# Performance work log

Measured on AMD Instinct MI355X. Metric: run time of the kernel, lower is better.

The kernel has to match this reference:

```python
import jax, jax.numpy as jnp
import numpy as np

B, S, C, V, LAT, NL = 256, 512, 256, 32, 256, 7
DILS = [1, 2, 4, 8, 16, 32, 64]
EPS = 1e-5


def setup_inputs() -> dict:
    key = jax.random.key(0)
    ks = jax.random.split(key, 24)
    s = 0.05
    inp = {
        "x": jax.random.randint(ks[0], (B, S), 0, V, dtype=jnp.int64 if jax.config.read("jax_enable_x64") else jnp.int32),
        "z": jax.random.normal(ks[1], (B, LAT), dtype=jnp.float32),
        "emb": jax.random.normal(ks[2], (V, C), dtype=jnp.float32) * s,
        "latent_W": jax.random.normal(ks[3], (LAT, C), dtype=jnp.float32) * s,
        "latent_b": jnp.zeros((C,), jnp.float32),
        "ln1_g": jnp.ones((NL, C), jnp.float32),
        "ln1_b": jnp.zeros((NL, C), jnp.float32),
        "w1": jax.random.normal(ks[4], (NL, C, C), jnp.float32) * s,
        "b1": jnp.zeros((NL, C), jnp.float32),
        "ln2_g": jnp.ones((NL, C), jnp.float32),
        "ln2_b": jnp.zeros((NL, C), jnp.float32),
        "wd": jax.random.normal(ks[5], (NL, 2, C, C), jnp.float32) * s,  # tap 0 = x[t-d], tap 1 = x[t]
        "bd": jnp.zeros((NL, C), jnp.float32),
        "ln3_g": jnp.ones((NL, C), jnp.float32),
        "ln3_b": jnp.zeros((NL, C), jnp.float32),
        "we": jax.random.normal(ks[6], (NL, C, C), jnp.float32) * s,
        "be": jnp.zeros((NL, C), jnp.float32),
        "wg": jax.random.normal(ks[7], (NL, C, C), jnp.float32) * s,
        "bg": jnp.zeros((NL, C), jnp.float32),
        "out_W": jax.random.normal(ks[8], (C, V), jnp.float32) * s,
        "out_b": jnp.zeros((V,), jnp.float32),
    }
    return inp


def _ln(h, g, b):
    mu = h.mean(-1, keepdims=True)
    var = jnp.mean((h - mu) ** 2, axis=-1, keepdims=True)
    return (h - mu) * jax.lax.rsqrt(var + EPS) * g + b


def _lrelu(h):
    return jnp.where(h >= 0, h, 0.01 * h)


def reference(x, z, emb, latent_W, latent_b, ln1_g, ln1_b, w1, b1,
              ln2_g, ln2_b, wd, bd, ln3_g, ln3_b, we, be, wg, bg,
              out_W, out_b):
    # channel-last layout [B, S, C] throughout (fuses away the torch transposes)
    h = emb[x] + (z @ latent_W + latent_b)[:, None, :]
    for i, d in enumerate(DILS):
        x_inp = h
        t = _lrelu(_ln(x_inp, ln1_g[i], ln1_b[i]))
        t = t @ w1[i] + b1[i]
        t = _lrelu(_ln(t, ln2_g[i], ln2_b[i]))
        # causal dilated conv, kernel=2: out[t] = W0*x[t-d] + W1*x[t]
        t_shift = jnp.pad(t, ((0, 0), (d, 0), (0, 0)))[:, :t.shape[1], :]
        t = t_shift @ wd[i, 0] + t @ wd[i, 1] + bd[i]
        t = _lrelu(_ln(t, ln3_g[i], ln3_b[i]))
        gated = (t @ we[i] + be[i]) * jax.nn.sigmoid(t @ wg[i] + bg[i])
        h = gated + x_inp
    logits = h @ out_W + out_b                      # [B, S, V]
    lp = jax.nn.log_softmax(logits, axis=-1)
    # gather log-prob of next token: lp[:, :-1, :] at x[:, 1:]
    return jnp.take_along_axis(lp[:, :-1, :], x[:, 1:, None], axis=2)[..., 0]
```

## Files before the change

### kernel.cpp

```cpp
#include <hip/hip_runtime.h>

typedef unsigned short u16;
typedef unsigned int   u32;
typedef __attribute__((ext_vector_type(8))) short short8;
typedef __attribute__((ext_vector_type(4))) float f32x4;

struct __align__(8) u16x4 { u16 x, y, z, w; };

#define NL 7
#define M_DIM 131072

#define VMW(N) asm volatile("s_waitcnt vmcnt(" #N ")" ::: "memory")
#define LGW()  asm volatile("s_waitcnt lgkmcnt(0)" ::: "memory")
#define BAR()  __builtin_amdgcn_s_barrier()

__device__ __forceinline__ float b2f(u16 u) {
  union { float f; u32 i; } c; c.i = ((u32)u) << 16; return c.f;
}
__device__ __forceinline__ u16 f2b(float f) {
  union { float f; u32 i; } c; c.f = f;
  u32 r = c.i + 0x7FFFu + ((c.i >> 16) & 1u);
  return (u16)(r >> 16);
}
__device__ __forceinline__ void gload16(const void* g, void* l) {
  __builtin_amdgcn_global_load_lds((const __attribute__((address_space(1))) void*)g,
                                   (__attribute__((address_space(3))) void*)l, 16, 0, 0);
}
__device__ __forceinline__ int xIdx(int row, int chunk) {
  return row * 256 + (((chunk) ^ (row & 7)) << 3);
}


__global__ __launch_bounds__(256) void conv_w1_k(const float* __restrict__ w1, u16* __restrict__ wT) {
  int idx = blockIdx.x * 256 + threadIdx.x;
  int i = idx >> 16, rem = idx & 65535;
  int n = rem >> 8, k = rem & 255;
  wT[idx] = f2b(w1[(i << 16) + (k << 8) + n]);
}

__global__ __launch_bounds__(256) void conv_wd_k(const float* __restrict__ wd, u16* __restrict__ wT) {
  int idx = blockIdx.x * 256 + threadIdx.x;
  int i = idx / 131072, rem = idx & 131071;
  int n = rem >> 9, k2 = rem & 511;
  int tap = k2 >> 8, k = k2 & 255;
  wT[idx] = f2b(wd[(((i * 2 + tap) << 8) + k) * 256 + n]);
}

__global__ __launch_bounds__(256) void conv_weg_k(const float* __restrict__ we, const float* __restrict__ wg,
                                                  u16* __restrict__ wT) {
  int idx = blockIdx.x * 256 + threadIdx.x;
  int i = idx / 131072, rem = idx & 131071;
  int src = rem >> 16, n = (rem >> 8) & 255, k = rem & 255;
  const float* W = src ? wg : we;
  wT[idx] = f2b(W[((i << 8) + k) * 256 + n]);
}

__global__ __launch_bounds__(256) void conv_wo_k(const float* __restrict__ outW, u16* __restrict__ wTo) {
  int idx = blockIdx.x * 256 + threadIdx.x;
  int v = idx >> 8, k = idx & 255;
  wTo[idx] = f2b(outW[k * 32 + v]);
}


__global__ __launch_bounds__(256) void zlat_k(const float* __restrict__ z, const float* __restrict__ W,
                                              const float* __restrict__ bias, float* __restrict__ zlat) {
  int b = blockIdx.x, c = threadIdx.x;
  float acc = bias[c];
  for (int l = 0; l < 256; ++l) acc += z[b * 256 + l] * W[l * 256 + c];
  zlat[b * 256 + c] = acc;
}


__global__ __launch_bounds__(256) void embed_k(const int* __restrict__ x, const float* __restrict__ emb,
                                               const float* __restrict__ zlat, u16* __restrict__ h) {
  int wave = threadIdx.x >> 6, lane = threadIdx.x & 63;
  int r = blockIdx.x * 4 + wave;
  int c = lane * 4;
  int tok = x[r];
  int bi = r >> 9;
  float4 ev = *(const float4*)&emb[tok * 256 + c];
  float4 zv = *(const float4*)&zlat[bi * 256 + c];
  u16x4 hb;
  hb.x = f2b(ev.x + zv.x); hb.y = f2b(ev.y + zv.y);
  hb.z = f2b(ev.z + zv.z); hb.w = f2b(ev.w + zv.w);
  *(u16x4*)&h[(long)r * 256 + c] = hb;
}


__global__ __launch_bounds__(256, 3) void gemm1_k(
    const u16* __restrict__ h, const u16* __restrict__ WT,
    const float* __restrict__ ln1g, const float* __restrict__ ln1b,
    const float* __restrict__ bias,
    const float* __restrict__ ln2g, const float* __restrict__ ln2b,
    u16* __restrict__ V)
{
  __shared__ __align__(16) u16 lA[64 * 256];
  __shared__ __align__(16) u16 lB[256 * 32];
  float* pS  = (float*)lB;
  float* pQ  = (float*)(lB + 512);
  float* muA = (float*)(lB + 1024);
  float* rsA = (float*)(lB + 1152);
  const int tid = threadIdx.x;
  const int lane = tid & 63;
  const int wv = tid >> 6;
  const int wc = wv * 64;
  const int m0 = blockIdx.x * 64;
  const int rA = tid >> 2;
  const int cSw = ((((tid & 3) - ((tid >> 3) & 3)) & 3)) * 8;
  const int lr = lane & 15;
  const int quad = lane >> 4;
  const int sw = ((quad + ((lr >> 1) & 3)) & 3) * 8;

  {
    const int half = lane >> 5, l5 = lane & 31;
    float4 ga = *(const float4*)&ln1g[l5 * 8];
    float4 gb = *(const float4*)&ln1g[l5 * 8 + 4];
    float4 ba = *(const float4*)&ln1b[l5 * 8];
    float4 bb = *(const float4*)&ln1b[l5 * 8 + 4];
    #pragma unroll 4
    for (int it = 0; it < 8; ++it) {
      int row = wv * 16 + it * 2 + half;
      uint4 hv = *(const uint4*)(h + (long)(m0 + row) * 256 + l5 * 8);
      float v0 = b2f((u16)(hv.x & 0xffff)), v1 = b2f((u16)(hv.x >> 16));
      float v2 = b2f((u16)(hv.y & 0xffff)), v3 = b2f((u16)(hv.y >> 16));
      float v4 = b2f((u16)(hv.z & 0xffff)), v5 = b2f((u16)(hv.z >> 16));
      float v6 = b2f((u16)(hv.w & 0xffff)), v7 = b2f((u16)(hv.w >> 16));
      float s = v0 + v1 + v2 + v3 + v4 + v5 + v6 + v7;
      float q = v0*v0 + v1*v1 + v2*v2 + v3*v3 + v4*v4 + v5*v5 + v6*v6 + v7*v7;
      #pragma unroll
      for (int o = 1; o < 32; o <<= 1) { s += __shfl_xor(s, o); q += __shfl_xor(q, o); }
      float mu = s * 0.00390625f;
      float var = q * 0.00390625f - mu * mu;
      float rs = rsqrtf(var + 1e-5f);
      float y0 = (v0 - mu) * rs * ga.x + ba.x; y0 = y0 >= 0.f ? y0 : 0.01f * y0;
      float y1 = (v1 - mu) * rs * ga.y + ba.y; y1 = y1 >= 0.f ? y1 : 0.01f * y1;
      float y2 = (v2 - mu) * rs * ga.z + ba.z; y2 = y2 >= 0.f ? y2 : 0.01f * y2;
      float y3 = (v3 - mu) * rs * ga.w + ba.w; y3 = y3 >= 0.f ? y3 : 0.01f * y3;
      float y4 = (v4 - mu) * rs * gb.x + bb.x; y4 = y4 >= 0.f ? y4 : 0.01f * y4;
      float y5 = (v5 - mu) * rs * gb.y + bb.y; y5 = y5 >= 0.f ? y5 : 0.01f * y5;
      float y6 = (v6 - mu) * rs * gb.z + bb.z; y6 = y6 >= 0.f ? y6 : 0.01f * y6;
      float y7 = (v7 - mu) * rs * gb.w + bb.w; y7 = y7 >= 0.f ? y7 : 0.01f * y7;
      uint4 ov;
      ov.x = (u32)f2b(y0) | ((u32)f2b(y1) << 16);
      ov.y = (u32)f2b(y2) | ((u32)f2b(y3) << 16);
      ov.z = (u32)f2b(y4) | ((u32)f2b(y5) << 16);
      ov.w = (u32)f2b(y6) | ((u32)f2b(y7) << 16);
      *(uint4*)&lA[xIdx(row, l5)] = ov;
    }
  }

  f32x4 acc[4][4];
  #pragma unroll
  for (int i = 0; i < 4; ++i)
    #pragma unroll
    for (int j = 0; j < 4; ++j) {
      acc[i][j][0] = 0.f; acc[i][j][1] = 0.f; acc[i][j][2] = 0.f; acc[i][j][3] = 0.f;
    }

  for (int kt = 0; kt < 8; ++kt) {
    const long bofs = (long)rA * 256 + kt * 32 + cSw;
    #pragma unroll
    for (int j = 0; j < 4; ++j)
      gload16(WT + bofs + (long)(64 * j) * 256, &lB[tid * 8 + j * 2048]);
    __syncthreads();

    short8 af[4], bfr[4];
    #pragma unroll
    for (int mt = 0; mt < 4; ++mt)
      af[mt] = *(const short8*)&lA[xIdx(mt * 16 + lr, 4 * kt + quad)];
    #pragma unroll
    for (int nt = 0; nt < 4; ++nt)
      bfr[nt] = *(const short8*)&lB[(wc + nt * 16 + lr) * 32 + sw];
    #pragma unroll
    for (int mt = 0; mt < 4; ++mt)
      #pragma unroll
      for (int nt = 0; nt < 4; ++nt)
        acc[mt][nt] = __builtin_amdgcn_mfma_f32_16x16x32_bf16(af[mt], bfr[nt], acc[mt][nt], 0, 0, 0);
    __syncthreads();
  }

  float biasv[4], gv[4], bv[4];
  #pragma unroll
  for (int nt = 0; nt < 4; ++nt) {
    int n = wc + nt * 16 + lr;
    biasv[nt] = bias[n]; gv[nt] = ln2g[n]; bv[nt] = ln2b[n];
  }
  #pragma unroll
  for (int mt = 0; mt < 4; ++mt)
    #pragma unroll
    for (int r = 0; r < 4; ++r) {
      float s = 0.f, q = 0.f;
      #pragma unroll
      for (int nt = 0; nt < 4; ++nt) {
        float v = acc[mt][nt][r] + biasv[nt];
        acc[mt][nt][r] = v;
        s += v; q += v * v;
      }
      #pragma unroll
      for (int o = 1; o < 16; o <<= 1) { s += __shfl_xor(s, o); q += __shfl_xor(q, o); }
      if (lr == 0) { pS[(mt * 16 + quad * 4 + r) * 4 + wv] = s; pQ[(mt * 16 + quad * 4 + r) * 4 + wv] = q; }
    }
  __syncthreads();
  if (tid < 64) {
    float S = pS[tid * 4 + 0] + pS[tid * 4 + 1] + pS[tid * 4 + 2] + pS[tid * 4 + 3];
    float Q = pQ[tid * 4 + 0] + pQ[tid * 4 + 1] + pQ[tid * 4 + 2] + pQ[tid * 4 + 3];
    float mu = S * 0.00390625f;
    float var = Q * 0.00390625f - mu * mu;
    muA[tid] = mu; rsA[tid] = rsqrtf(var + 1e-5f);
  }
  __syncthreads();
  #pragma unroll
  for (int mt = 0; mt < 4; ++mt)
    #pragma unroll
    for (int r = 0; r < 4; ++r) {
      int row = mt * 16 + quad * 4 + r;
      float mu = muA[row], rs = rsA[row];
      #pragma unroll
      for (int nt = 0; nt < 4; ++nt) {
        float y = (acc[mt][nt][r] - mu) * rs * gv[nt] + bv[nt];
        y = y >= 0.f ? y : 0.01f * y;
        V[(long)(m0 + row) * 256 + wc + nt * 16 + lr] = f2b(y);
      }
    }
}


__global__ __launch_bounds__(512, 2) void conv_gate_k(
    const u16* __restrict__ A,
    const u16* __restrict__ WTd,
    int dil,
    const float* __restrict__ bd3, const float* __restrict__ g3, const float* __restrict__ bb3,
    const u16* __restrict__ WTe, const u16* __restrict__ WTg,
    const float* __restrict__ bev_, const float* __restrict__ bgv_,
    u16* __restrict__ h)
{
  __shared__ __align__(16) u16 pT[128 * 256];
  __shared__ __align__(16) u16 stg[2][12288];
  float* pS  = (float*)stg[0];
  float* pQ  = (float*)(stg[0] + 1024);
  float* muA = (float*)(stg[0] + 2048);
  float* rsA = (float*)(stg[0] + 2304);

  const int tid = threadIdx.x;
  const int lane = tid & 63;
  const int wv = tid >> 6;
  const int mw = wv >> 2;
  const int nw = wv & 3;
  const int rb = mw * 64;
  const int wc = nw * 64;
  const int m0 = blockIdx.x * 128;
  const int rA = tid >> 2;
  const int cSw = ((((tid & 3) - ((tid >> 3) & 3)) & 3)) * 8;
  const int lr = lane & 15;
  const int quad = lane >> 4;
  const int sw = ((quad + ((lr >> 1) & 3)) & 3) * 8;
  const int mm = m0 + rA;
  const int s1 = mm & 511;
  const short8 zero8 = {0, 0, 0, 0, 0, 0, 0, 0};

  bool zz[4];
  #pragma unroll
  for (int mt = 0; mt < 4; ++mt)
    zz[mt] = ((m0 + rb + mt * 16 + lr) & 511) < dil;

#define STAGE1(KT, BB) do {                                                   \
    const int kt_ = (KT);                                                     \
    const int kk_ = (kt_ & 7) * 32;                                           \
    const int rr_ = (kt_ < 8 && s1 >= dil) ? (mm - dil) : mm;                 \
    gload16(A + (long)rr_ * 256 + kk_ + cSw, &stg[BB][tid * 8]);              \
    const u16* bS_ = WTd + kt_ * 32 + cSw;                                    \
    gload16(bS_ + (long)rA * 512,         &stg[BB][4096 + tid * 8]);          \
    gload16(bS_ + (long)(rA + 128) * 512, &stg[BB][8192 + tid * 8]);          \
  } while (0)
#define STAGEW(WP, KT, BB) do {                                               \
    const long bofs_ = (long)rA * 256 + (KT) * 32 + cSw;                      \
    gload16((WP) + bofs_,              &stg[BB][4096 + tid * 8]);             \
    gload16((WP) + bofs_ + 128L * 256, &stg[BB][8192 + tid * 8]);             \
  } while (0)

  f32x4 acc[4][4];
  #pragma unroll
  for (int i = 0; i < 4; ++i)
    #pragma unroll
    for (int j = 0; j < 4; ++j) {
      acc[i][j][0] = 0.f; acc[i][j][1] = 0.f; acc[i][j][2] = 0.f; acc[i][j][3] = 0.f;
    }

  STAGE1(0, 0);
  STAGE1(1, 1);
  VMW(3);
  BAR();

  #pragma unroll
  for (int r = 0; r < 16; ++r) {
    const int bb = r & 1;
    short8 af[4], bfr[4];
    #pragma unroll
    for (int mt = 0; mt < 4; ++mt) {
      af[mt] = *(const short8*)&stg[bb][(rb + mt * 16 + lr) * 32 + sw];
      if (r < 8 && zz[mt]) af[mt] = zero8;
    }
    #pragma unroll
    for (int nt = 0; nt < 4; ++nt)
      bfr[nt] = *(const short8*)&stg[bb][4096 + (wc + nt * 16 + lr) * 32 + sw];
    LGW();
    BAR();
    if (r <= 13)      STAGE1(r + 2, bb);
    else if (r == 14) STAGEW(WTe, 0, 0);
    else              STAGEW(WTe, 1, 1);
    #pragma unroll
    for (int mt = 0; mt < 4; ++mt)
      #pragma unroll
      for (int nt = 0; nt < 4; ++nt)
        acc[mt][nt] = __builtin_amdgcn_mfma_f32_16x16x32_bf16(af[mt], bfr[nt], acc[mt][nt], 0, 0, 0);
    if (r <= 13)      VMW(3);
    else if (r == 14) VMW(2);
    BAR();
  }

  float b3v[4], g3v[4], o3v[4];
  #pragma unroll
  for (int nt = 0; nt < 4; ++nt) {
    int n = wc + nt * 16 + lr;
    b3v[nt] = bd3[n]; g3v[nt] = g3[n]; o3v[nt] = bb3[n];
  }
  #pragma unroll
  for (int mt = 0; mt < 4; ++mt)
    #pragma unroll
    for (int r = 0; r < 4; ++r) {
      float s = 0.f, q = 0.f;
      #pragma unroll
      for (int nt = 0; nt < 4; ++nt) {
        float v = acc[mt][nt][r] + b3v[nt];
        acc[mt][nt][r] = v;
        s += v; q += v * v;
      }
      #pragma unroll
      for (int o = 1; o < 16; o <<= 1) { s += __shfl_xor(s, o); q += __shfl_xor(q, o); }
      if (lr == 0) {
        int row = rb + mt * 16 + quad * 4 + r;
        pS[row * 4 + nw] = s; pQ[row * 4 + nw] = q;
      }
    }
  LGW(); BAR();
  if (tid < 128) {
    float S = pS[tid * 4 + 0] + pS[tid * 4 + 1] + pS[tid * 4 + 2] + pS[tid * 4 + 3];
    float Q = pQ[tid * 4 + 0] + pQ[tid * 4 + 1] + pQ[tid * 4 + 2] + pQ[tid * 4 + 3];
    float mu = S * 0.00390625f;
    float var = Q * 0.00390625f - mu * mu;
    muA[tid] = mu; rsA[tid] = rsqrtf(var + 1e-5f);
  }
  LGW(); BAR();
  #pragma unroll
  for (int mt = 0; mt < 4; ++mt)
    #pragma unroll
    for (int r = 0; r < 4; ++r) {
      int row = rb + mt * 16 + quad * 4 + r;
      float mu = muA[row], rs = rsA[row];
      #pragma unroll
      for (int nt = 0; nt < 4; ++nt) {
        int col = wc + nt * 16 + lr;
        float y = (acc[mt][nt][r] - mu) * rs * g3v[nt] + o3v[nt];
        y = y >= 0.f ? y : 0.01f * y;
        pT[xIdx(row, col >> 3) + (col & 7)] = f2b(y);
      }
    }
  LGW(); VMW(2); BAR();

  f32x4 accE[4][4], accG[4][4];
  #pragma unroll
  for (int i = 0; i < 4; ++i)
    #pragma unroll
    for (int j = 0; j < 4; ++j) {
      accE[i][j][0] = 0.f; accE[i][j][1] = 0.f; accE[i][j][2] = 0.f; accE[i][j][3] = 0.f;
      accG[i][j][0] = 0.f; accG[i][j][1] = 0.f; accG[i][j][2] = 0.f; accG[i][j][3] = 0.f;
    }

  #pragma unroll
  for (int k = 0; k < 8; ++k) {
    const int bb = k & 1;
    short8 paf[4], bfe[4];
    #pragma unroll
    for (int mt = 0; mt < 4; ++mt)
      paf[mt] = *(const short8*)&pT[xIdx(rb + mt * 16 + lr, 4 * k + quad)];
    #pragma unroll
    for (int nt = 0; nt < 4; ++nt)
      bfe[nt] = *(const short8*)&stg[bb][4096 + (wc + nt * 16 + lr) * 32 + sw];
    LGW(); BAR();
    if (k <= 5)      STAGEW(WTe, k + 2, bb);
    else if (k == 6) STAGEW(WTg, 0, 0);
    else             STAGEW(WTg, 1, 1);
    #pragma unroll
    for (int mt = 0; mt < 4; ++mt)
      #pragma unroll
      for (int nt = 0; nt < 4; ++nt)
        accE[mt][nt] = __builtin_amdgcn_mfma_f32_16x16x32_bf16(paf[mt], bfe[nt], accE[mt][nt], 0, 0, 0);
    VMW(2);
    BAR();
  }

  #pragma unroll
  for (int k = 0; k < 8; ++k) {
    const int bb = k & 1;
    short8 paf[4], bfg[4];
    #pragma unroll
    for (int mt = 0; mt < 4; ++mt)
      paf[mt] = *(const short8*)&pT[xIdx(rb + mt * 16 + lr, 4 * k + quad)];
    #pragma unroll
    for (int nt = 0; nt < 4; ++nt)
      bfg[nt] = *(const short8*)&stg[bb][4096 + (wc + nt * 16 + lr) * 32 + sw];
    LGW(); BAR();
    if (k <= 5) STAGEW(WTg, k + 2, bb);
    #pragma unroll
    for (int mt = 0; mt < 4; ++mt)
      #pragma unroll
      for (int nt = 0; nt < 4; ++nt)
        accG[mt][nt] = __builtin_amdgcn_mfma_f32_16x16x32_bf16(paf[mt], bfg[nt], accG[mt][nt], 0, 0, 0);
    if (k <= 5)      VMW(2);
    else if (k == 6) VMW(0);
    if (k <= 6) BAR();
  }

  float bev[4], bgv[4];
  #pragma unroll
  for (int nt = 0; nt < 4; ++nt) {
    int n = wc + nt * 16 + lr;
    bev[nt] = bev_[n]; bgv[nt] = bgv_[n];
  }
  #pragma unroll
  for (int mt = 0; mt < 4; ++mt)
    #pragma unroll
    for (int r = 0; r < 4; ++r) {
      int row = rb + mt * 16 + quad * 4 + r;
      long off = (long)(m0 + row) * 256;
      #pragma unroll
      for (int nt = 0; nt < 4; ++nt) {
        int n = wc + nt * 16 + lr;
        float e = accE[mt][nt][r] + bev[nt];
        float gg = accG[mt][nt][r] + bgv[nt];
        float hn = e * (1.f / (1.f + expf(-gg))) + b2f(h[off + n]);
        h[off + n] = f2b(hn);
      }
    }
#undef STAGE1
#undef STAGEW
}


__global__ __launch_bounds__(256) void final_k(const u16* __restrict__ h, const u16* __restrict__ WTo,
                                               const float* __restrict__ outb, const int* __restrict__ x,
                                               float* __restrict__ out) {
  __shared__ u16 lW[32 * 264];
  const int tid = threadIdx.x;
  const int lane = tid & 63;
  const int wv = tid >> 6;
  const int mBase = blockIdx.x * 256 + wv * 64;

  #pragma unroll
  for (int j = 0; j < 4; ++j) {
    int chunk = tid + 256 * j;
    int v = chunk >> 5, k8 = chunk & 31;
    uint4 w4 = *(const uint4*)(WTo + v * 256 + k8 * 8);
    *(uint4*)&lW[v * 264 + k8 * 8] = w4;
  }
  __syncthreads();

  const int lq = (lane >> 4) * 8;
  const int lr = lane & 15;
  const int quad = lane >> 4;

  f32x4 acc[4][2];
  #pragma unroll
  for (int mt = 0; mt < 4; ++mt) {
    acc[mt][0][0] = 0.f; acc[mt][0][1] = 0.f; acc[mt][0][2] = 0.f; acc[mt][0][3] = 0.f;
    acc[mt][1][0] = 0.f; acc[mt][1][1] = 0.f; acc[mt][1][2] = 0.f; acc[mt][1][3] = 0.f;
  }

  for (int kt = 0; kt < 8; ++kt) {
    short8 bf0 = *(const short8*)&lW[lr * 264 + kt * 32 + lq];
    short8 bf1 = *(const short8*)&lW[(16 + lr) * 264 + kt * 32 + lq];
    #pragma unroll
    for (int mt = 0; mt < 4; ++mt) {
      short8 af = *(const short8*)(h + (long)(mBase + mt * 16 + lr) * 256 + kt * 32 + lq);
      acc[mt][0] = __builtin_amdgcn_mfma_f32_16x16x32_bf16(af, bf0, acc[mt][0], 0, 0, 0);
      acc[mt][1] = __builtin_amdgcn_mfma_f32_16x16x32_bf16(af, bf1, acc[mt][1], 0, 0, 0);
    }
  }

  float ob0 = outb[lr], ob1 = outb[16 + lr];
  #pragma unroll
  for (int mt = 0; mt < 4; ++mt)
    #pragma unroll
    for (int r = 0; r < 4; ++r) {
      int row = mBase + mt * 16 + quad * 4 + r;
      float lo = acc[mt][0][r] + ob0;
      float hi = acc[mt][1][r] + ob1;
      float mx = fmaxf(lo, hi);
      #pragma unroll
      for (int o = 1; o < 16; o <<= 1) mx = fmaxf(mx, __shfl_xor(mx, o));
      float se = expf(lo - mx) + expf(hi - mx);
      #pragma unroll
      for (int o = 1; o < 16; o <<= 1) se += __shfl_xor(se, o);
      int s = row & 511;
      int xa = (s == 511) ? row : (row + 1);
      int tok = x[xa];
      float lg = (tok < 16) ? lo : hi;
      float lp = lg - mx - logf(se);
      if (s != 511 && lr == (tok & 15))
        out[(row >> 9) * 511 + s] = lp;
    }
}


extern "C" void kernel_launch(void* const* d_in, const int* in_sizes, int n_in,
                              void* d_out, int out_size, void* d_ws, size_t ws_size,
                              hipStream_t stream) {
  const int*   x    = (const int*)d_in[0];
  const float* z    = (const float*)d_in[1];
  const float* emb  = (const float*)d_in[2];
  const float* latW = (const float*)d_in[3];
  const float* latb = (const float*)d_in[4];
  const float* ln1g = (const float*)d_in[5];
  const float* ln1b = (const float*)d_in[6];
  const float* w1   = (const float*)d_in[7];
  const float* b1   = (const float*)d_in[8];
  const float* ln2g = (const float*)d_in[9];
  const float* ln2b = (const float*)d_in[10];
  const float* wd   = (const float*)d_in[11];
  const float* bd   = (const float*)d_in[12];
  const float* ln3g = (const float*)d_in[13];
  const float* ln3b = (const float*)d_in[14];
  const float* we   = (const float*)d_in[15];
  const float* be   = (const float*)d_in[16];
  const float* wg   = (const float*)d_in[17];
  const float* bg   = (const float*)d_in[18];
  const float* outW = (const float*)d_in[19];
  const float* outb = (const float*)d_in[20];

  char* ws = (char*)d_ws;
  u16*   h    = (u16*)(ws + 0);
  u16*   bufA = (u16*)(ws + 67108864);
  float* zlat = (float*)(ws + 201326592);
  u16*   wT1  = (u16*)(ws + 201588736);
  u16*   wTd  = (u16*)(ws + 202506240);
  u16*   wTeg = (u16*)(ws + 204341248);
  u16*   wTo  = (u16*)(ws + 206176256);

  conv_w1_k <<<1792, 256, 0, stream>>>(w1, wT1);
  conv_wd_k <<<3584, 256, 0, stream>>>(wd, wTd);
  conv_weg_k<<<3584, 256, 0, stream>>>(we, wg, wTeg);
  conv_wo_k <<<32, 256, 0, stream>>>(outW, wTo);
  zlat_k    <<<256, 256, 0, stream>>>(z, latW, latb, zlat);
  embed_k   <<<M_DIM / 4, 256, 0, stream>>>(x, emb, zlat, h);

  for (int i = 0; i < NL; ++i) {
    int d = 1 << i;
    gemm1_k<<<M_DIM / 64, 256, 0, stream>>>(
        h, wT1 + i * 65536, ln1g + i * 256, ln1b + i * 256, b1 + i * 256,
        ln2g + i * 256, ln2b + i * 256, bufA);
    conv_gate_k<<<M_DIM / 128, 512, 0, stream>>>(
        bufA, wTd + i * 131072, d,
        bd + i * 256, ln3g + i * 256, ln3b + i * 256,
        wTeg + i * 131072, wTeg + i * 131072 + 65536,
        be + i * 256, bg + i * 256, h);
  }

  final_k<<<M_DIM / 256, 256, 0, stream>>>(h, wTo, outb, x, (float*)d_out);
}
```

Baseline: 1.411 ms.

## Fuse gemm1 into conv-gate kernel with halo recompute and ping-pong h buffers

Merges the per-layer gemm1 kernel into the conv/gate kernel. Each 128-row block recomputes LN1+GEMM1+LN2 for 192 rows (a 64-row halo covering the dilated tap) and keeps the result in LDS, so the intermediate activation never round-trips through global memory. The residual stream ping-pongs between two buffers, because neighbouring blocks read halo rows of the input. This cuts global traffic and kernel launches, at the cost of 50% redundant GEMM1 work, more LDS (lower occupancy risk), and clamped halo rows at sequence starts.

```diff
diff --git a/kernel.cpp b/kernel.cpp
--- a/kernel.cpp
+++ b/kernel.cpp
@@ -13,6 +13,7 @@
 #define VMW(N) asm volatile("s_waitcnt vmcnt(" #N ")" ::: "memory")
 #define LGW()  asm volatile("s_waitcnt lgkmcnt(0)" ::: "memory")
 #define BAR()  __builtin_amdgcn_s_barrier()
+#define MFMA   __builtin_amdgcn_mfma_f32_16x16x32_bf16
 
 __device__ __forceinline__ float b2f(u16 u) {
   union { float f; u32 i; } c; c.i = ((u32)u) << 16; return c.f;
@@ -87,166 +88,29 @@
 }
 
 
-__global__ __launch_bounds__(256, 3) void gemm1_k(
-    const u16* __restrict__ h, const u16* __restrict__ WT,
+__global__ __launch_bounds__(512, 2) void layer_k(
+    const u16* __restrict__ hIn,
+    u16* __restrict__ hOut,
+    const u16* __restrict__ W1,
     const float* __restrict__ ln1g, const float* __restrict__ ln1b,
-    const float* __restrict__ bias,
+    const float* __restrict__ b1,
     const float* __restrict__ ln2g, const float* __restrict__ ln2b,
-    u16* __restrict__ V)
-{
-  __shared__ __align__(16) u16 lA[64 * 256];
-  __shared__ __align__(16) u16 lB[256 * 32];
-  float* pS  = (float*)lB;
-  float* pQ  = (float*)(lB + 512);
-  float* muA = (float*)(lB + 1024);
-  float* rsA = (float*)(lB + 1152);
-  const int tid = threadIdx.x;
-  const int lane = tid & 63;
-  const int wv = tid >> 6;
-  const int wc = wv * 64;
-  const int m0 = blockIdx.x * 64;
-  const int rA = tid >> 2;
-  const int cSw = ((((tid & 3) - ((tid >> 3) & 3)) & 3)) * 8;
-  const int lr = lane & 15;
-  const int quad = lane >> 4;
-  const int sw = ((quad + ((lr >> 1) & 3)) & 3) * 8;
-
-  {
-    const int half = lane >> 5, l5 = lane & 31;
-    float4 ga = *(const float4*)&ln1g[l5 * 8];
-    float4 gb = *(const float4*)&ln1g[l5 * 8 + 4];
-    float4 ba = *(const float4*)&ln1b[l5 * 8];
-    float4 bb = *(const float4*)&ln1b[l5 * 8 + 4];
-    #pragma unroll 4
-    for (int it = 0; it < 8; ++it) {
-      int row = wv * 16 + it * 2 + half;
-      uint4 hv = *(const uint4*)(h + (long)(m0 + row) * 256 + l5 * 8);
-      float v0 = b2f((u16)(hv.x & 0xffff)), v1 = b2f((u16)(hv.x >> 16));
-      float v2 = b2f((u16)(hv.y & 0xffff)), v3 = b2f((u16)(hv.y >> 16));
-      float v4 = b2f((u16)(hv.z & 0xffff)), v5 = b2f((u16)(hv.z >> 16));
-      float v6 = b2f((u16)(hv.w & 0xffff)), v7 = b2f((u16)(hv.w >> 16));
-      float s = v0 + v1 + v2 + v3 + v4 + v5 + v6 + v7;
-      float q = v0*v0 + v1*v1 + v2*v2 + v3*v3 + v4*v4 + v5*v5 + v6*v6 + v7*v7;
-      #pragma unroll
-      for (int o = 1; o < 32; o <<= 1) { s += __shfl_xor(s, o); q += __shfl_xor(q, o); }
-      float mu = s * 0.00390625f;
-      float var = q * 0.00390625f - mu * mu;
-      float rs = rsqrtf(var + 1e-5f);
-      float y0 = (v0 - mu) * rs * ga.x + ba.x; y0 = y0 >= 0.f ? y0 : 0.01f * y0;
-      float y1 = (v1 - mu) * rs * ga.y + ba.y; y1 = y1 >= 0.f ? y1 : 0.01f * y1;
-      float y2 = (v2 - mu) * rs * ga.z + ba.z; y2 = y2 >= 0.f ? y2 : 0.01f * y2;
-      float y3 = (v3 - mu) * rs * ga.w + ba.w; y3 = y3 >= 0.f ? y3 : 0.01f * y3;
-      float y4 = (v4 - mu) * rs * gb.x + bb.x; y4 = y4 >= 0.f ? y4 : 0.01f * y4;
-      float y5 = (v5 - mu) * rs * gb.y + bb.y; y5 = y5 >= 0.f ? y5 : 0.01f * y5;
-      float y6 = (v6 - mu) * rs * gb.z + bb.z; y6 = y6 >= 0.f ? y6 : 0.01f * y6;
-      float y7 = (v7 - mu) * rs * gb.w + bb.w; y7 = y7 >= 0.f ? y7 : 0.01f * y7;
-      uint4 ov;
-      ov.x = (u32)f2b(y0) | ((u32)f2b(y1) << 16);
-      ov.y = (u32)f2b(y2) | ((u32)f2b(y3) << 16);
-      ov.z = (u32)f2b(y4) | ((u32)f2b(y5) << 16);
-      ov.w = (u32)f2b(y6) | ((u32)f2b(y7) << 16);
-      *(uint4*)&lA[xIdx(row, l5)] = ov;
-    }
-  }
-
-  f32x4 acc[4][4];
-  #pragma unroll
-  for (int i = 0; i < 4; ++i)
-    #pragma unroll
-    for (int j = 0; j < 4; ++j) {
-      acc[i][j][0] = 0.f; acc[i][j][1] = 0.f; acc[i][j][2] = 0.f; acc[i][j][3] = 0.f;
-    }
-
-  for (int kt = 0; kt < 8; ++kt) {
-    const long bofs = (long)rA * 256 + kt * 32 + cSw;
-    #pragma unroll
-    for (int j = 0; j < 4; ++j)
-      gload16(WT + bofs + (long)(64 * j) * 256, &lB[tid * 8 + j * 2048]);
-    __syncthreads();
-
-    short8 af[4], bfr[4];
-    #pragma unroll
-    for (int mt = 0; mt < 4; ++mt)
-      af[mt] = *(const short8*)&lA[xIdx(mt * 16 + lr, 4 * kt + quad)];
-    #pragma unroll
-    for (int nt = 0; nt < 4; ++nt)
-      bfr[nt] = *(const short8*)&lB[(wc + nt * 16 + lr) * 32 + sw];
-    #pragma unroll
-    for (int mt = 0; mt < 4; ++mt)
-      #pragma unroll
-      for (int nt = 0; nt < 4; ++nt)
-        acc[mt][nt] = __builtin_amdgcn_mfma_f32_16x16x32_bf16(af[mt], bfr[nt], acc[mt][nt], 0, 0, 0);
-    __syncthreads();
-  }
-
-  float biasv[4], gv[4], bv[4];
-  #pragma unroll
-  for (int nt = 0; nt < 4; ++nt) {
-    int n = wc + nt * 16 + lr;
-    biasv[nt] = bias[n]; gv[nt] = ln2g[n]; bv[nt] = ln2b[n];
-  }
-  #pragma unroll
-  for (int mt = 0; mt < 4; ++mt)
-    #pragma unroll
-    for (int r = 0; r < 4; ++r) {
-      float s = 0.f, q = 0.f;
-      #pragma unroll
-      for (int nt = 0; nt < 4; ++nt) {
-        float v = acc[mt][nt][r] + biasv[nt];
-        acc[mt][nt][r] = v;
-        s += v; q += v * v;
-      }
-      #pragma unroll
-      for (int o = 1; o < 16; o <<= 1) { s += __shfl_xor(s, o); q += __shfl_xor(q, o); }
-      if (lr == 0) { pS[(mt * 16 + quad * 4 + r) * 4 + wv] = s; pQ[(mt * 16 + quad * 4 + r) * 4 + wv] = q; }
-    }
-  __syncthreads();
-  if (tid < 64) {
-    float S = pS[tid * 4 + 0] + pS[tid * 4 + 1] + pS[tid * 4 + 2] + pS[tid * 4 + 3];
-    float Q = pQ[tid * 4 + 0] + pQ[tid * 4 + 1] + pQ[tid * 4 + 2] + pQ[tid * 4 + 3];
-    float mu = S * 0.00390625f;
-    float var = Q * 0.00390625f - mu * mu;
-    muA[tid] = mu; rsA[tid] = rsqrtf(var + 1e-5f);
-  }
-  __syncthreads();
-  #pragma unroll
-  for (int mt = 0; mt < 4; ++mt)
-    #pragma unroll
-    for (int r = 0; r < 4; ++r) {
-      int row = mt * 16 + quad * 4 + r;
-      float mu = muA[row], rs = rsA[row];
-      #pragma unroll
-      for (int nt = 0; nt < 4; ++nt) {
-        float y = (acc[mt][nt][r] - mu) * rs * gv[nt] + bv[nt];
-        y = y >= 0.f ? y : 0.01f * y;
-        V[(long)(m0 + row) * 256 + wc + nt * 16 + lr] = f2b(y);
-      }
-    }
-}
-
-
-__global__ __launch_bounds__(512, 2) void conv_gate_k(
-    const u16* __restrict__ A,
     const u16* __restrict__ WTd,
     int dil,
     const float* __restrict__ bd3, const float* __restrict__ g3, const float* __restrict__ bb3,
     const u16* __restrict__ WTe, const u16* __restrict__ WTg,
-    const float* __restrict__ bev_, const float* __restrict__ bgv_,
-    u16* __restrict__ h)
+    const float* __restrict__ bev_, const float* __restrict__ bgv_)
 {
-  __shared__ __align__(16) u16 pT[128 * 256];
-  __shared__ __align__(16) u16 stg[2][12288];
-  float* pS  = (float*)stg[0];
-  float* pQ  = (float*)(stg[0] + 1024);
-  float* muA = (float*)(stg[0] + 2048);
-  float* rsA = (float*)(stg[0] + 2304);
+  __shared__ __align__(16) u16 big[192 * 256];
+  __shared__ __align__(16) u16 stg[2][8192];
+  __shared__ float pS[192][4], pQ[192][4];
+  __shared__ float muA[192], rsA[192];
 
   const int tid = threadIdx.x;
   const int lane = tid & 63;
   const int wv = tid >> 6;
   const int mw = wv >> 2;
   const int nw = wv & 3;
-  const int rb = mw * 64;
   const int wc = nw * 64;
   const int m0 = blockIdx.x * 128;
   const int rA = tid >> 2;
@@ -254,30 +118,163 @@
   const int lr = lane & 15;
   const int quad = lane >> 4;
   const int sw = ((quad + ((lr >> 1) & 3)) & 3) * 8;
-  const int mm = m0 + rA;
-  const int s1 = mm & 511;
   const short8 zero8 = {0, 0, 0, 0, 0, 0, 0, 0};
 
+  const u16* pW1 = W1 + (long)rA * 256 + cSw;
+  const u16* pWd = WTd + (long)rA * 512 + cSw;
+  const u16* pWe = WTe + (long)rA * 256 + cSw;
+  const u16* pWg = WTg + (long)rA * 256 + cSw;
+
+  auto ST_G1 = [&](int kt, int bb) {
+    gload16(pW1 + kt * 32,             &stg[bb][tid * 8]);
+    gload16(pW1 + 128 * 256 + kt * 32, &stg[bb][4096 + tid * 8]);
+  };
+  auto ST_WD = [&](int kt, int bb) {
+    gload16(pWd + kt * 32,             &stg[bb][tid * 8]);
+    gload16(pWd + 128 * 512 + kt * 32, &stg[bb][4096 + tid * 8]);
+  };
+  auto ST_WE = [&](int kt, int bb) {
+    gload16(pWe + kt * 32,             &stg[bb][tid * 8]);
+    gload16(pWe + 128 * 256 + kt * 32, &stg[bb][4096 + tid * 8]);
+  };
+  auto ST_WG = [&](int kt, int bb) {
+    gload16(pWg + kt * 32,             &stg[bb][tid * 8]);
+    gload16(pWg + 128 * 256 + kt * 32, &stg[bb][4096 + tid * 8]);
+  };
+  auto rdW = [&](int bb, int nt) -> short8 {
+    return *(const short8*)&stg[bb][(wc + nt * 16 + lr) * 32 + sw];
+  };
+
+  ST_G1(0, 0);
+  ST_G1(1, 1);
+
+  {
+    const int half = lane >> 5, l5 = lane & 31;
+    float4 ga = *(const float4*)&ln1g[l5 * 8];
+    float4 gb = *(const float4*)&ln1g[l5 * 8 + 4];
+    float4 ba = *(const float4*)&ln1b[l5 * 8];
+    float4 bbv = *(const float4*)&ln1b[l5 * 8 + 4];
+    #pragma unroll 4
+    for (int it = 0; it < 12; ++it) {
+      int j = wv * 24 + it * 2 + half;
+      int g = m0 - 64 + j;
+      if (g < 0) g = 0;
+      uint4 hv = *(const uint4*)(hIn + (long)g * 256 + l5 * 8);
+      float v0 = b2f((u16)(hv.x & 0xffff)), v1 = b2f((u16)(hv.x >> 16));
+      float v2 = b2f((u16)(hv.y & 0xffff)), v3 = b2f((u16)(hv.y >> 16));
+      float v4 = b2f((u16)(hv.z & 0xffff)), v5 = b2f((u16)(hv.z >> 16));
+      float v6 = b2f((u16)(hv.w & 0xffff)), v7 = b2f((u16)(hv.w >> 16));
+      float s = v0 + v1 + v2 + v3 + v4 + v5 + v6 + v7;
+      float q = v0*v0 + v1*v1 + v2*v2 + v3*v3 + v4*v4 + v5*v5 + v6*v6 + v7*v7;
+      #pragma unroll
+      for (int o = 1; o < 32; o <<= 1) { s += __shfl_xor(s, o); q += __shfl_xor(q, o); }
+      float mu = s * 0.00390625f;
+      float var = q * 0.00390625f - mu * mu;
+      float rs = rsqrtf(var + 1e-5f);
+      float y0 = (v0 - mu) * rs * ga.x + ba.x;  y0 = y0 >= 0.f ? y0 : 0.01f * y0;
+      float y1 = (v1 - mu) * rs * ga.y + ba.y;  y1 = y1 >= 0.f ? y1 : 0.01f * y1;
+      float y2 = (v2 - mu) * rs * ga.z + ba.z;  y2 = y2 >= 0.f ? y2 : 0.01f * y2;
+      float y3 = (v3 - mu) * rs * ga.w + ba.w;  y3 = y3 >= 0.f ? y3 : 0.01f * y3;
+      float y4 = (v4 - mu) * rs * gb.x + bbv.x; y4 = y4 >= 0.f ? y4 : 0.01f * y4;
+      float y5 = (v5 - mu) * rs * gb.y + bbv.y; y5 = y5 >= 0.f ? y5 : 0.01f * y5;
+      float y6 = (v6 - mu) * rs * gb.z + bbv.z; y6 = y6 >= 0.f ? y6 : 0.01f * y6;
+      float y7 = (v7 - mu) * rs * gb.w + bbv.w; y7 = y7 >= 0.f ? y7 : 0.01f * y7;
+      uint4 ov;
+      ov.x = (u32)f2b(y0) | ((u32)f2b(y1) << 16);
+      ov.y = (u32)f2b(y2) | ((u32)f2b(y3) << 16);
+      ov.z = (u32)f2b(y4) | ((u32)f2b(y5) << 16);
+      ov.w = (u32)f2b(y6) | ((u32)f2b(y7) << 16);
+      *(uint4*)&big[xIdx(j, l5)] = ov;
+    }
+  }
+  LGW(); VMW(2); BAR();
+
+  f32x4 acc1[6][4];
+  #pragma unroll
+  for (int i = 0; i < 6; ++i)
+    #pragma unroll
+    for (int j = 0; j < 4; ++j) {
+      acc1[i][j][0] = 0.f; acc1[i][j][1] = 0.f; acc1[i][j][2] = 0.f; acc1[i][j][3] = 0.f;
+    }
+
+  #pragma unroll
+  for (int t = 0; t < 8; ++t) {
+    const int bb = t & 1;
+    short8 af[6], bf[4];
+    #pragma unroll
+    for (int mt = 0; mt < 6; ++mt)
+      af[mt] = *(const short8*)&big[xIdx(mw * 96 + mt * 16 + lr, 4 * t + quad)];
+    #pragma unroll
+    for (int nt = 0; nt < 4; ++nt) bf[nt] = rdW(bb, nt);
+    LGW(); BAR();
+    if (t <= 5)      ST_G1(t + 2, bb);
+    else if (t == 6) ST_WD(0, 0);
+    else             ST_WD(1, 1);
+    #pragma unroll
+    for (int mt = 0; mt < 6; ++mt)
+      #pragma unroll
+      for (int nt = 0; nt < 4; ++nt)
+        acc1[mt][nt] = MFMA(af[mt], bf[nt], acc1[mt][nt], 0, 0, 0);
+    VMW(2); BAR();
+  }
+
+  {
+    float bv[4], gv[4], ov[4];
+    #pragma unroll
+    for (int nt = 0; nt < 4; ++nt) {
+      int n = wc + nt * 16 + lr;
+      bv[nt] = b1[n]; gv[nt] = ln2g[n]; ov[nt] = ln2b[n];
+    }
+    #pragma unroll
+    for (int mt = 0; mt < 6; ++mt)
+      #pragma unroll
+      for (int r = 0; r < 4; ++r) {
+        float s = 0.f, q = 0.f;
+        #pragma unroll
+        for (int nt = 0; nt < 4; ++nt) {
+          float v = acc1[mt][nt][r] + bv[nt];
+          acc1[mt][nt][r] = v;
+          s += v; q += v * v;
+        }
+        #pragma unroll
+        for (int o = 1; o < 16; o <<= 1) { s += __shfl_xor(s, o); q += __shfl_xor(q, o); }
+        if (lr == 0) {
+          int row = mw * 96 + mt * 16 + quad * 4 + r;
+          pS[row][nw] = s; pQ[row][nw] = q;
+        }
+      }
+    LGW(); BAR();
+    if (tid < 192) {
+      float S = pS[tid][0] + pS[tid][1] + pS[tid][2] + pS[tid][3];
+      float Q = pQ[tid][0] + pQ[tid][1] + pQ[tid][2] + pQ[tid][3];
+      float mu = S * 0.00390625f;
+      float var = Q * 0.00390625f - mu * mu;
+      muA[tid] = mu; rsA[tid] = rsqrtf(var + 1e-5f);
+    }
+    LGW(); BAR();
+    #pragma unroll
+    for (int mt = 0; mt < 6; ++mt)
+      #pragma unroll
+      for (int r = 0; r < 4; ++r) {
+        int row = mw * 96 + mt * 16 + quad * 4 + r;
+        float mu = muA[row], rs = rsA[row];
+        #pragma unroll
+        for (int nt = 0; nt < 4; ++nt) {
+          int col = wc + nt * 16 + lr;
+          float y = (acc1[mt][nt][r] - mu) * rs * gv[nt] + ov[nt];
+          y = y >= 0.f ? y : 0.01f * y;
+          big[xIdx(row, col >> 3) + (col & 7)] = f2b(y);
+        }
+      }
+    LGW(); BAR();
+  }
+
+  const int rb = mw * 64;
   bool zz[4];
   #pragma unroll
   for (int mt = 0; mt < 4; ++mt)
     zz[mt] = ((m0 + rb + mt * 16 + lr) & 511) < dil;
 
-#define STAGE1(KT, BB) do {                                                   \
-    const int kt_ = (KT);                                                     \
-    const int kk_ = (kt_ & 7) * 32;                                           \
-    const int rr_ = (kt_ < 8 && s1 >= dil) ? (mm - dil) : mm;                 \
-    gload16(A + (long)rr_ * 256 + kk_ + cSw, &stg[BB][tid * 8]);              \
-    const u16* bS_ = WTd + kt_ * 32 + cSw;                                    \
-    gload16(bS_ + (long)rA * 512,         &stg[BB][4096 + tid * 8]);          \
-    gload16(bS_ + (long)(rA + 128) * 512, &stg[BB][8192 + tid * 8]);          \
-  } while (0)
-#define STAGEW(WP, KT, BB) do {                                               \
-    const long bofs_ = (long)rA * 256 + (KT) * 32 + cSw;                      \
-    gload16((WP) + bofs_,              &stg[BB][4096 + tid * 8]);             \
-    gload16((WP) + bofs_ + 128L * 256, &stg[BB][8192 + tid * 8]);             \
-  } while (0)
-
   f32x4 acc[4][4];
   #pragma unroll
   for (int i = 0; i < 4; ++i)
@@ -286,86 +283,82 @@
       acc[i][j][0] = 0.f; acc[i][j][1] = 0.f; acc[i][j][2] = 0.f; acc[i][j][3] = 0.f;
     }
 
-  STAGE1(0, 0);
-  STAGE1(1, 1);
-  VMW(3);
-  BAR();
-
-  #pragma unroll
-  for (int r = 0; r < 16; ++r) {
-    const int bb = r & 1;
-    short8 af[4], bfr[4];
+  #pragma unroll
+  for (int t = 0; t < 16; ++t) {
+    const int bb = t & 1;
+    const bool tap0 = t < 8;
+    const int kc = t & 7;
+    short8 af[4], bf[4];
     #pragma unroll
     for (int mt = 0; mt < 4; ++mt) {
-      af[mt] = *(const short8*)&stg[bb][(rb + mt * 16 + lr) * 32 + sw];
-      if (r < 8 && zz[mt]) af[mt] = zero8;
-    }
-    #pragma unroll
-    for (int nt = 0; nt < 4; ++nt)
-      bfr[nt] = *(const short8*)&stg[bb][4096 + (wc + nt * 16 + lr) * 32 + sw];
-    LGW();
-    BAR();
-    if (r <= 13)      STAGE1(r + 2, bb);
-    else if (r == 14) STAGEW(WTe, 0, 0);
-    else              STAGEW(WTe, 1, 1);
+      int j = 64 + rb + mt * 16 + lr - (tap0 ? dil : 0);
+      af[mt] = *(const short8*)&big[xIdx(j, 4 * kc + quad)];
+      if (tap0 && zz[mt]) af[mt] = zero8;
+    }
+    #pragma unroll
+    for (int nt = 0; nt < 4; ++nt) bf[nt] = rdW(bb, nt);
+    LGW(); BAR();
+    if (t <= 13)      ST_WD(t + 2, bb);
+    else if (t == 14) ST_WE(0, 0);
+    else              ST_WE(1, 1);
     #pragma unroll
     for (int mt = 0; mt < 4; ++mt)
       #pragma unroll
       for (int nt = 0; nt < 4; ++nt)
-        acc[mt][nt] = __builtin_amdgcn_mfma_f32_16x16x32_bf16(af[mt], bfr[nt], acc[mt][nt], 0, 0, 0);
-    if (r <= 13)      VMW(3);
-    else if (r == 14) VMW(2);
-    BAR();
-  }
-
-  float b3v[4], g3v[4], o3v[4];
-  #pragma unroll
-  for (int nt = 0; nt < 4; ++nt) {
-    int n = wc + nt * 16 + lr;
-    b3v[nt] = bd3[n]; g3v[nt] = g3[n]; o3v[nt] = bb3[n];
-  }
-  #pragma unroll
-  for (int mt = 0; mt < 4; ++mt)
-    #pragma unroll
-    for (int r = 0; r < 4; ++r) {
-      float s = 0.f, q = 0.f;
-      #pragma unroll
-      for (int nt = 0; nt < 4; ++nt) {
-        float v = acc[mt][nt][r] + b3v[nt];
-        acc[mt][nt][r] = v;
-        s += v; q += v * v;
+        acc[mt][nt] = MFMA(af[mt], bf[nt], acc[mt][nt], 0, 0, 0);
+    VMW(2); BAR();
+  }
+
+  {
+    float bv[4], gv[4], ov[4];
+    #pragma unroll
+    for (int nt = 0; nt < 4; ++nt) {
+      int n = wc + nt * 16 + lr;
+      bv[nt] = bd3[n]; gv[nt] = g3[n]; ov[nt] = bb3[n];
+    }
+    #pragma unroll
+    for (int mt = 0; mt < 4; ++mt)
+      #pragma unroll
+      for (int r = 0; r < 4; ++r) {
+        float s = 0.f, q = 0.f;
+        #pragma unroll
+        for (int nt = 0; nt < 4; ++nt) {
+          float v = acc[mt][nt][r] + bv[nt];
+          acc[mt][nt][r] = v;
+          s += v; q += v * v;
+        }
+        #pragma unroll
+        for (int o = 1; o < 16; o <<= 1) { s += __shfl_xor(s, o); q += __shfl_xor(q, o); }
+        if (lr == 0) {
+          int row = rb + mt * 16 + quad * 4 + r;
+          pS[row][nw] = s; pQ[row][nw] = q;
+        }
       }
-      #pragma unroll
-      for (int o = 1; o < 16; o <<= 1) { s += __shfl_xor(s, o); q += __shfl_xor(q, o); }
-      if (lr == 0) {
+    LGW(); BAR();
+    if (tid < 128) {
+      float S = pS[tid][0] + pS[tid][1] + pS[tid][2] + pS[tid][3];
+      float Q = pQ[tid][0] + pQ[tid][1] + pQ[tid][2] + pQ[tid][3];
+      float mu = S * 0.00390625f;
+      float var = Q * 0.00390625f - mu * mu;
+      muA[tid] = mu; rsA[tid] = rsqrtf(var + 1e-5f);
+    }
+    LGW(); BAR();
+    #pragma unroll
+    for (int mt = 0; mt < 4; ++mt)
+      #pragma unroll
+      for (int r = 0; r < 4; ++r) {
         int row = rb + mt * 16 + quad * 4 + r;
-        pS[row * 4 + nw] = s; pQ[row * 4 + nw] = q;
+        float mu = muA[row], rs = rsA[row];
+        #pragma unroll
+        for (int nt = 0; nt < 4; ++nt) {
+          int col = wc + nt * 16 + lr;
+          float y = (acc[mt][nt][r] - mu) * rs * gv[nt] + ov[nt];
+          y = y >= 0.f ? y : 0.01f * y;
+          big[xIdx(row, col >> 3) + (col & 7)] = f2b(y);
+        }
       }
-    }
-  LGW(); BAR();
-  if (tid < 128) {
-    float S = pS[tid * 4 + 0] + pS[tid * 4 + 1] + pS[tid * 4 + 2] + pS[tid * 4 + 3];
-    float Q = pQ[tid * 4 + 0] + pQ[tid * 4 + 1] + pQ[tid * 4 + 2] + pQ[tid * 4 + 3];
-    float mu = S * 0.00390625f;
-    float var = Q * 0.00390625f - mu * mu;
-    muA[tid] = mu; rsA[tid] = rsqrtf(var + 1e-5f);
-  }
-  LGW(); BAR();
-  #pragma unroll
-  for (int mt = 0; mt < 4; ++mt)
-    #pragma unroll
-    for (int r = 0; r < 4; ++r) {
-      int row = rb + mt * 16 + quad * 4 + r;
-      float mu = muA[row], rs = rsA[row];
-      #pragma unroll
-      for (int nt = 0; nt < 4; ++nt) {
-        int col = wc + nt * 16 + lr;
-        float y = (acc[mt][nt][r] - mu) * rs * g3v[nt] + o3v[nt];
-        y = y >= 0.f ? y : 0.01f * y;
-        pT[xIdx(row, col >> 3) + (col & 7)] = f2b(y);
-      }
-    }
-  LGW(); VMW(2); BAR();
+    LGW(); BAR();
+  }
 
   f32x4 accE[4][4], accG[4][4];
   #pragma unroll
@@ -379,43 +372,39 @@
   #pragma unroll
   for (int k = 0; k < 8; ++k) {
     const int bb = k & 1;
-    short8 paf[4], bfe[4];
-    #pragma unroll
-    for (int mt = 0; mt < 4; ++mt)
-      paf[mt] = *(const short8*)&pT[xIdx(rb + mt * 16 + lr, 4 * k + quad)];
-    #pragma unroll
-    for (int nt = 0; nt < 4; ++nt)
-      bfe[nt] = *(const short8*)&stg[bb][4096 + (wc + nt * 16 + lr) * 32 + sw];
-    LGW(); BAR();
-    if (k <= 5)      STAGEW(WTe, k + 2, bb);
-    else if (k == 6) STAGEW(WTg, 0, 0);
-    else             STAGEW(WTg, 1, 1);
+    short8 pf[4], bf[4];
+    #pragma unroll
+    for (int mt = 0; mt < 4; ++mt)
+      pf[mt] = *(const short8*)&big[xIdx(rb + mt * 16 + lr, 4 * k + quad)];
+    #pragma unroll
+    for (int nt = 0; nt < 4; ++nt) bf[nt] = rdW(bb, nt);
+    LGW(); BAR();
+    if (k <= 5)      ST_WE(k + 2, bb);
+    else if (k == 6) ST_WG(0, 0);
+    else             ST_WG(1, 1);
     #pragma unroll
     for (int mt = 0; mt < 4; ++mt)
       #pragma unroll
       for (int nt = 0; nt < 4; ++nt)
-        accE[mt][nt] = __builtin_amdgcn_mfma_f32_16x16x32_bf16(paf[mt], bfe[nt], accE[mt][nt], 0, 0, 0);
-    VMW(2);
-    BAR();
-  }
-
+        accE[mt][nt] = MFMA(pf[mt], bf[nt], accE[mt][nt], 0, 0, 0);
+    VMW(2); BAR();
+  }
   #pragma unroll
   for (int k = 0; k < 8; ++k) {
     const int bb = k & 1;
-    short8 paf[4], bfg[4];
-    #pragma unroll
-    for (int mt = 0; mt < 4; ++mt)
-      paf[mt] = *(const short8*)&pT[xIdx(rb + mt * 16 + lr, 4 * k + quad)];
-    #pragma unroll
-    for (int nt = 0; nt < 4; ++nt)
-      bfg[nt] = *(const short8*)&stg[bb][4096 + (wc + nt * 16 + lr) * 32 + sw];
-    LGW(); BAR();
-    if (k <= 5) STAGEW(WTg, k + 2, bb);
+    short8 pf[4], bf[4];
+    #pragma unroll
+    for (int mt = 0; mt < 4; ++mt)
+      pf[mt] = *(const short8*)&big[xIdx(rb + mt * 16 + lr, 4 * k + quad)];
+    #pragma unroll
+    for (int nt = 0; nt < 4; ++nt) bf[nt] = rdW(bb, nt);
+    LGW(); BAR();
+    if (k <= 5) ST_WG(k + 2, bb);
     #pragma unroll
     for (int mt = 0; mt < 4; ++mt)
       #pragma unroll
       for (int nt = 0; nt < 4; ++nt)
-        accG[mt][nt] = __builtin_amdgcn_mfma_f32_16x16x32_bf16(paf[mt], bfg[nt], accG[mt][nt], 0, 0, 0);
+        accG[mt][nt] = MFMA(pf[mt], bf[nt], accG[mt][nt], 0, 0, 0);
     if (k <= 5)      VMW(2);
     else if (k == 6) VMW(0);
     if (k <= 6) BAR();
@@ -438,12 +427,10 @@
         int n = wc + nt * 16 + lr;
         float e = accE[mt][nt][r] + bev[nt];
         float gg = accG[mt][nt][r] + bgv[nt];
-        float hn = e * (1.f / (1.f + expf(-gg))) + b2f(h[off + n]);
-        h[off + n] = f2b(hn);
+        float hn = e * (1.f / (1.f + expf(-gg))) + b2f(hIn[off + n]);
+        hOut[off + n] = f2b(hn);
       }
     }
-#undef STAGE1
-#undef STAGEW
 }
 
 
@@ -482,8 +469,8 @@
     #pragma unroll
     for (int mt = 0; mt < 4; ++mt) {
       short8 af = *(const short8*)(h + (long)(mBase + mt * 16 + lr) * 256 + kt * 32 + lq);
-      acc[mt][0] = __builtin_amdgcn_mfma_f32_16x16x32_bf16(af, bf0, acc[mt][0], 0, 0, 0);
-      acc[mt][1] = __builtin_amdgcn_mfma_f32_16x16x32_bf16(af, bf1, acc[mt][1], 0, 0, 0);
+      acc[mt][0] = MFMA(af, bf0, acc[mt][0], 0, 0, 0);
+      acc[mt][1] = MFMA(af, bf1, acc[mt][1], 0, 0, 0);
     }
   }
 
@@ -538,8 +525,8 @@
   const float* outb = (const float*)d_in[20];
 
   char* ws = (char*)d_ws;
-  u16*   h    = (u16*)(ws + 0);
-  u16*   bufA = (u16*)(ws + 67108864);
+  u16*   h0   = (u16*)(ws + 0);
+  u16*   h1   = (u16*)(ws + 67108864);
   float* zlat = (float*)(ws + 201326592);
   u16*   wT1  = (u16*)(ws + 201588736);
   u16*   wTd  = (u16*)(ws + 202506240);
@@ -551,19 +538,21 @@
   conv_weg_k<<<3584, 256, 0, stream>>>(we, wg, wTeg);
   conv_wo_k <<<32, 256, 0, stream>>>(outW, wTo);
   zlat_k    <<<256, 256, 0, stream>>>(z, latW, latb, zlat);
-  embed_k   <<<M_DIM / 4, 256, 0, stream>>>(x, emb, zlat, h);
+  embed_k   <<<M_DIM / 4, 256, 0, stream>>>(x, emb, zlat, h0);
 
   for (int i = 0; i < NL; ++i) {
     int d = 1 << i;
-    gemm1_k<<<M_DIM / 64, 256, 0, stream>>>(
-        h, wT1 + i * 65536, ln1g + i * 256, ln1b + i * 256, b1 + i * 256,
-        ln2g + i * 256, ln2b + i * 256, bufA);
-    conv_gate_k<<<M_DIM / 128, 512, 0, stream>>>(
-        bufA, wTd + i * 131072, d,
+    const u16* hIn = (i & 1) ? h1 : h0;
+    u16*       hOut = (i & 1) ? h0 : h1;
+    layer_k<<<M_DIM / 128, 512, 0, stream>>>(
+        hIn, hOut, wT1 + i * 65536,
+        ln1g + i * 256, ln1b + i * 256, b1 + i * 256,
+        ln2g + i * 256, ln2b + i * 256,
+        wTd + i * 131072, d,
         bd + i * 256, ln3g + i * 256, ln3b + i * 256,
         wTeg + i * 131072, wTeg + i * 131072 + 65536,
-        be + i * 256, bg + i * 256, h);
-  }
-
-  final_k<<<M_DIM / 256, 256, 0, stream>>>(h, wTo, outb, x, (float*)d_out);
-}
+        be + i * 256, bg + i * 256);
+  }
+
+  final_k<<<M_DIM / 256, 256, 0, stream>>>(h1, wTo, outb, x, (float*)d_out);
+}
```

New measurement: 1.505 ms. 1.07x slower.
